# Optimization experiments

Hardware: AMD Instinct MI355X
Metric: run time of the kernel (lower is better)

## Reference

```python
import jax, jax.numpy as jnp
import numpy as np
from jax import lax

S, T, I, H = 50, 2048, 64, 256  # num_series, seq_len, input_size, hidden_size

def _xavier(key, shape):
    fan_in, fan_out = shape[-1], shape[-2]
    b = np.sqrt(6.0 / (fan_in + fan_out)).astype(np.float32)
    return jax.random.uniform(key, shape, jnp.float32, -b, b)

def setup_inputs() -> dict:
    key = jax.random.key(0)
    ks = jax.random.split(key, 6)
    return {
        "input_data": jax.random.normal(ks[0], (S, T, 1 + I), jnp.float32),
        "hidden": jnp.zeros((S, H), jnp.float32),
        "fixed_effects": jax.random.normal(ks[1], (S, T), jnp.float32),
        "W_ih": _xavier(ks[2], (S, H, I)),
        "W_hh": _xavier(ks[3], (S, H, H)),
        "b_ih": jnp.zeros((S, H), jnp.float32),
        "b_hh": jnp.zeros((S, H), jnp.float32),
        "W_lin": _xavier(ks[4], (S, 1, H)),
        "b_lin": jnp.zeros((S, 1), jnp.float32),
        "gaussian_likelihood": 1,
        "prediction": 0,
    }

def reference(input_data, hidden, fixed_effects, W_ih, W_hh, b_ih, b_hh, W_lin, b_lin, gaussian_likelihood, prediction):
    z = input_data[:, :, 0]          # [S, T] targets
    x = input_data[:, :, 1:]         # [S, T, I] RNN inputs

    # All 50 per-series Elman RNNs run as one batched scan over time.
    def step(h, x_t):                # h: [S, H], x_t: [S, I]
        h = jnp.tanh(jnp.einsum('shi,si->sh', W_ih, x_t) + b_ih
                     + jnp.einsum('shg,sg->sh', W_hh, h) + b_hh)
        return h, h

    xs = jnp.swapaxes(x, 0, 1)       # [T, S, I]
    _, hs = lax.scan(step, hidden, xs)
    rnn_out = jnp.swapaxes(hs, 0, 1)  # [S, T, H]

    # Per-series linear head (output_size=1) then abs -> sigma [S, T]
    sig = jnp.einsum('sth,sh->st', rnn_out, W_lin[:, 0, :]) + b_lin
    sigma = jnp.abs(sig)

    if prediction == 0:
        # Gaussian log-likelihood: log N(z-f; 0, sigma) - log N(0; 0, sigma)
        # = -(z - f)^2 / (2 sigma^2), summed over all elements.
        diff = z - fixed_effects
        log_lik = jnp.sum(-(diff * diff) / (2.0 * sigma * sigma))
        return (log_lik, sigma)
    else:
        # r ~ N(0, sigma) elementwise, u = f + r, softmax over time axis.
        eps = jax.random.normal(jax.random.key(1), sigma.shape, sigma.dtype)
        u = fixed_effects + sigma * eps
        return jax.nn.softmax(u, axis=1)
```

## Files before the change

kernel.cpp:

```cpp
#include <hip/hip_runtime.h>
#include <cmath>

#define S_CNT 50
#define T_CNT 2048
#define I_DIM 64
#define H_DIM 256
#define CHK   8
#define NCHK  (T_CNT / CHK)

typedef float vf2 __attribute__((ext_vector_type(2)));

__device__ __forceinline__ float fast_tanh(float x) {
    float e = __expf(2.0f * x);
    return 1.0f - __fdividef(2.0f, e + 1.0f);
}

__device__ __forceinline__ vf2 pkfma(vf2 a, vf2 b, vf2 c) {
#if __has_builtin(__builtin_elementwise_fma)
    return __builtin_elementwise_fma(a, b, c);
#else
    vf2 r; r.x = fmaf(a.x, b.x, c.x); r.y = fmaf(a.y, b.y, c.y); return r;
#endif
}

__device__ __forceinline__ float fma4(const float4 w, const float4 h, float a) {
    a = fmaf(w.x, h.x, a);
    a = fmaf(w.y, h.y, a);
    a = fmaf(w.z, h.z, a);
    a = fmaf(w.w, h.w, a);
    return a;
}

template <int CTRL>
__device__ __forceinline__ float dpp_xadd(float x) {
    const int xi = __float_as_int(x);
    const int yi = __builtin_amdgcn_update_dpp(xi, xi, CTRL, 0xF, 0xF, false);
    return x + __int_as_float(yi);
}

__device__ __forceinline__ void lds_barrier() {
    __builtin_amdgcn_sched_barrier(0);
    asm volatile("s_waitcnt lgkmcnt(0)");
    __builtin_amdgcn_s_barrier();
    __builtin_amdgcn_sched_barrier(0);
}

__launch_bounds__(256, 4)
__global__ void precompute_u_kernel(const float* __restrict__ input_data,
                                    const float* __restrict__ W_ih,
                                    const float* __restrict__ b_ih,
                                    const float* __restrict__ b_hh,
                                    float* __restrict__ U)
{
    const int s  = blockIdx.x;
    const int tb = blockIdx.y;
    const int j  = threadIdx.x;

    float4 w[16];
    const float4* wrow =
        reinterpret_cast<const float4*>(W_ih + ((size_t)s * H_DIM + j) * I_DIM);
#pragma unroll
    for (int k = 0; k < 16; ++k) w[k] = wrow[k];
    const float bsum = b_ih[s * H_DIM + j] + b_hh[s * H_DIM + j];

    __shared__ float xs[32][I_DIM];
    const float* inb = input_data + (size_t)s * T_CNT * 65;
    float* Ub = U + (size_t)s * T_CNT * H_DIM;

    const int t0 = tb * 32;
    for (int idx = j; idx < 32 * I_DIM; idx += 256) {
        const int row = idx >> 6, col = idx & 63;
        xs[row][col] = inb[(size_t)(t0 + row) * 65 + 1 + col];
    }
    __syncthreads();
    for (int tt = 0; tt < 32; ++tt) {
        const float4* xv = reinterpret_cast<const float4*>(&xs[tt][0]);
        float a0 = bsum, a1 = 0.f, a2 = 0.f, a3 = 0.f;
#pragma unroll
        for (int k = 0; k < 16; k += 4) {
            a0 = fma4(w[k],     xv[k],     a0);
            a1 = fma4(w[k + 1], xv[k + 1], a1);
            a2 = fma4(w[k + 2], xv[k + 2], a2);
            a3 = fma4(w[k + 3], xv[k + 3], a3);
        }
        Ub[(size_t)(t0 + tt) * H_DIM + j] = (a0 + a1) + (a2 + a3);
    }
}

__global__
__launch_bounds__(512)
__attribute__((amdgpu_waves_per_eu(1, 2)))
void rnn_main9(const float* __restrict__ hidden,
               const float* __restrict__ W_hh,
               float* __restrict__ U)
{
    const int s    = blockIdx.x;
    const int tid  = threadIdx.x;
    const int g    = tid >> 3;
    const int p    = tid & 7;

    const int s1 = (p ^ (p >> 2)) & 1;
    const int s2 = (p ^ (p >> 1)) & 1;
    const int jr = s1 + 2 * s2;
    const int jown = 4 * g + jr;

    __shared__ __align__(16) float hA[H_DIM];
    __shared__ __align__(16) float hB[H_DIM];

    if (tid < H_DIM) hA[tid] = hidden[s * H_DIM + tid];

    vf2 w2[4][16];
#pragma unroll
    for (int r = 0; r < 4; ++r) {
        const float4* wrow = reinterpret_cast<const float4*>(
            W_hh + ((size_t)s * H_DIM + 4 * g + r) * H_DIM);
#pragma unroll
        for (int m = 0; m < 8; ++m) {
            const float4 wv = wrow[8 * m + p];
            w2[r][2 * m]     = vf2{wv.x, wv.y};
            w2[r][2 * m + 1] = vf2{wv.z, wv.w};
        }
    }

    float* Ub = U + (size_t)s * T_CNT * H_DIM;
    float* us = Ub + jown;

    const float* u0 = Ub + jown;
    float cu0 = u0[0 * H_DIM], cu1 = u0[1 * H_DIM];
    float cu2 = u0[2 * H_DIM], cu3 = u0[3 * H_DIM];
    float cu4 = u0[4 * H_DIM], cu5 = u0[5 * H_DIM];
    float cu6 = u0[6 * H_DIM], cu7 = u0[7 * H_DIM];
    const float* up = Ub + jown + CHK * H_DIM;

    const bool wsel = (p < 4);
    const bool sel1 = (s1 != 0);
    const bool sel2 = (s2 != 0);

    __syncthreads();

#define RNN_STEP(HRD, HWR, UVAL)                                              \
    {                                                                         \
        const float4* hv = reinterpret_cast<const float4*>(HRD);              \
        vf2 a0 = vf2{0.f, 0.f}, b0 = vf2{0.f, 0.f};                           \
        vf2 a1 = vf2{0.f, 0.f}, b1 = vf2{0.f, 0.f};                           \
        vf2 a2 = vf2{0.f, 0.f}, b2 = vf2{0.f, 0.f};                           \
        vf2 a3 = vf2{0.f, 0.f}, b3 = vf2{0.f, 0.f};                           \
        _Pragma("unroll")                                                     \
        for (int m = 0; m < 8; ++m) {                                         \
            const float4 h4 = hv[8 * m + p];                                  \
            const vf2 hlo = vf2{h4.x, h4.y};                                  \
            const vf2 hhi = vf2{h4.z, h4.w};                                  \
            a0 = pkfma(w2[0][2 * m], hlo, a0);                                \
            b0 = pkfma(w2[0][2 * m + 1], hhi, b0);                            \
            a1 = pkfma(w2[1][2 * m], hlo, a1);                                \
            b1 = pkfma(w2[1][2 * m + 1], hhi, b1);                            \
            a2 = pkfma(w2[2][2 * m], hlo, a2);                                \
            b2 = pkfma(w2[2][2 * m + 1], hhi, b2);                            \
            a3 = pkfma(w2[3][2 * m], hlo, a3);                                \
            b3 = pkfma(w2[3][2 * m + 1], hhi, b3);                            \
        }                                                                     \
        const vf2 s0v = a0 + b0, s1v = a1 + b1;                               \
        const vf2 s2v = a2 + b2, s3v = a3 + b3;                               \
        const float d0 = s0v.x + s0v.y, d1 = s1v.x + s1v.y;                   \
        const float d2 = s2v.x + s2v.y, d3 = s3v.x + s3v.y;                   \
                                                         \
        const float e0 = dpp_xadd<0xB1>(d0);                                  \
        const float e1 = dpp_xadd<0xB1>(d1);                                  \
        const float e2 = dpp_xadd<0xB1>(d2);                                  \
        const float e3 = dpp_xadd<0xB1>(d3);                                  \
                        \
        const float c0 = sel1 ? e1 : e0;                                      \
        const float c1 = sel1 ? e3 : e2;                                      \
                                                         \
        const float f0 = dpp_xadd<0x4E>(c0);                                  \
        const float f1 = dpp_xadd<0x4E>(c1);                                  \
                               \
        const float gg = sel2 ? f1 : f0;                                      \
                  \
        const float fr = dpp_xadd<0x141>(gg);                                 \
        const float hval = fast_tanh(fr + (UVAL));                            \
        if (wsel) { (HWR)[jown] = hval; *us = hval; }                         \
        us += H_DIM;                                                          \
        lds_barrier();                                                        \
    }

    for (int c = 0; c < NCHK; ++c) {
        const float nx0 = up[0 * H_DIM], nx1 = up[1 * H_DIM];
        const float nx2 = up[2 * H_DIM], nx3 = up[3 * H_DIM];
        const float nx4 = up[4 * H_DIM], nx5 = up[5 * H_DIM];
        const float nx6 = up[6 * H_DIM], nx7 = up[7 * H_DIM];

        RNN_STEP(hA, hB, cu0)
        RNN_STEP(hB, hA, cu1)
        RNN_STEP(hA, hB, cu2)
        RNN_STEP(hB, hA, cu3)
        RNN_STEP(hA, hB, cu4)
        RNN_STEP(hB, hA, cu5)
        RNN_STEP(hA, hB, cu6)
        RNN_STEP(hB, hA, cu7)

        cu0 = nx0; cu1 = nx1; cu2 = nx2; cu3 = nx3;
        cu4 = nx4; cu5 = nx5; cu6 = nx6; cu7 = nx7;
        if (c < NCHK - 2) up += CHK * H_DIM;
    }
#undef RNN_STEP
}

__launch_bounds__(256, 4)
__global__ void finalize_kernel(const float* __restrict__ input_data,
                                const float* __restrict__ fe,
                                const float* __restrict__ W_lin,
                                const float* __restrict__ b_lin,
                                const float* __restrict__ H,
                                float* __restrict__ out)
{
    const int s    = blockIdx.x;
    const int tb   = blockIdx.y;
    const int tid  = threadIdx.x;
    const int wave = tid >> 6;
    const int lane = tid & 63;

    const float4 wl =
        reinterpret_cast<const float4*>(W_lin + s * H_DIM)[lane];
    const float blin = b_lin[s];
    const float* Hb  = H + (size_t)s * T_CNT * H_DIM;
    const float* inb = input_data + (size_t)s * T_CNT * 65;
    const float* feb = fe + (size_t)s * T_CNT;
    float* sig_out   = out + 1 + (size_t)s * T_CNT;

    float ll = 0.f;
    for (int i = 0; i < 128; ++i) {
        const int t = tb * 512 + 4 * i + wave;
        const float4 h4 =
            reinterpret_cast<const float4*>(Hb + (size_t)t * H_DIM)[lane];
        float d = fma4(wl, h4, 0.f);
#pragma unroll
        for (int m = 1; m <= 32; m <<= 1) d += __shfl_xor(d, m);
        const float sigma = fabsf(d + blin);
        if (lane == 0) {
            sig_out[t] = sigma;
            const float diff = inb[(size_t)t * 65] - feb[t];
            ll -= (diff * diff) / (2.f * sigma * sigma);
        }
    }
    __shared__ float red[4];
    if (lane == 0) red[wave] = ll;
    __syncthreads();
    if (tid == 0) atomicAdd(out, (red[0] + red[1]) + (red[2] + red[3]));
}

__launch_bounds__(1024, 4)
__global__ void rnn_fallback_kernel(const float* __restrict__ input_data,
                                    const float* __restrict__ hidden,
                                    const float* __restrict__ fe,
                                    const float* __restrict__ W_ih,
                                    const float* __restrict__ W_hh,
                                    const float* __restrict__ b_ih,
                                    const float* __restrict__ b_hh,
                                    const float* __restrict__ W_lin,
                                    const float* __restrict__ b_lin,
                                    float* __restrict__ out)
{
    const int s    = blockIdx.x;
    const int tid  = threadIdx.x;
    const int j    = tid >> 2;
    const int q    = tid & 3;
    const int lane = tid & 63;
    const int wv   = tid >> 6;

    __shared__ float hbuf[2][H_DIM];
    __shared__ float zbuf[T_CNT];
    __shared__ float febuf[T_CNT];
    __shared__ float wlin_lds[H_DIM];
    __shared__ float wsum[2][16];
    __shared__ float xbuf[64][I_DIM];

    const float* in_base = input_data + (size_t)s * T_CNT * 65;
    const float* fe_base = fe + (size_t)s * T_CNT;

    for (int t = tid; t < T_CNT; t += 1024) {
        zbuf[t]  = in_base[(size_t)t * 65];
        febuf[t] = fe_base[t];
    }
    if (tid < H_DIM) {
        hbuf[1][tid]  = hidden[s * H_DIM + tid];
        wlin_lds[tid] = W_lin[s * H_DIM + tid];
    }

    float4 w[16];
    {
        const float4* wrow =
            reinterpret_cast<const float4*>(W_hh + ((size_t)s * H_DIM + j) * H_DIM);
#pragma unroll
        for (int m = 0; m < 16; ++m) w[m] = wrow[4 * m + q];
    }
    float4 wx[4];
    {
        const float4* wxrow =
            reinterpret_cast<const float4*>(W_ih + ((size_t)s * H_DIM + j) * I_DIM);
#pragma unroll
        for (int m = 0; m < 4; ++m) wx[m] = wxrow[4 * m + q];
    }
    const float badd = b_ih[s * H_DIM + j] + b_hh[s * H_DIM + j];
    const float blin = b_lin[s];
    float* sig_out = out + 1 + (size_t)s * T_CNT;

    float ll = 0.f, sv_prev = 0.f;
    __syncthreads();

    for (int c = 0; c < T_CNT / 64; ++c) {
        for (int idx = tid; idx < 64 * I_DIM; idx += 1024) {
            const int row = idx >> 6, col = idx & 63;
            xbuf[row][col] = in_base[(size_t)(c * 64 + row) * 65 + 1 + col];
        }
        __syncthreads();
        for (int tt = 0; tt < 64; ++tt) {
            const int t  = c * 64 + tt;
            const int rp = (t + 1) & 1;
            {
                float sv = sv_prev;
                sv += __shfl_xor(sv, 4);
                sv += __shfl_xor(sv, 8);
                sv += __shfl_xor(sv, 16);
                sv += __shfl_xor(sv, 32);
                if (lane == 0) wsum[(t - 1) & 1][wv] = sv;
            }
            if (tid == 0 && t >= 2) {
                const int tm = t - 2;
                const float* wp = wsum[tm & 1];
                float sg = (((wp[0] + wp[1]) + (wp[2] + wp[3])) +
                            ((wp[4] + wp[5]) + (wp[6] + wp[7]))) +
                           (((wp[8] + wp[9]) + (wp[10] + wp[11])) +
                            ((wp[12] + wp[13]) + (wp[14] + wp[15]))) + blin;
                const float sigma = fabsf(sg);
                sig_out[tm] = sigma;
                const float diff = zbuf[tm] - febuf[tm];
                ll -= (diff * diff) / (2.f * sigma * sigma);
            }
            const float4* hv = reinterpret_cast<const float4*>(&hbuf[rp][0]);
            float a0 = 0.f, a1 = 0.f, a2 = 0.f, a3 = 0.f;
#pragma unroll
            for (int m = 0; m < 16; m += 4) {
                a0 = fma4(w[m],     hv[4 * (m + 0) + q], a0);
                a1 = fma4(w[m + 1], hv[4 * (m + 1) + q], a1);
                a2 = fma4(w[m + 2], hv[4 * (m + 2) + q], a2);
                a3 = fma4(w[m + 3], hv[4 * (m + 3) + q], a3);
            }
            const float4* xv = reinterpret_cast<const float4*>(&xbuf[tt][0]);
#pragma unroll
            for (int m = 0; m < 4; ++m) a0 = fma4(wx[m], xv[4 * m + q], a0);

            float dot = (a0 + a1) + (a2 + a3);
            dot += __shfl_xor(dot, 1);
            dot += __shfl_xor(dot, 2);
            const float h = fast_tanh(dot + badd);
            if (q == 0) hbuf[t & 1][j] = h;
            sv_prev = h * wlin_lds[j];
            __syncthreads();
        }
        __syncthreads();
    }
    {
        float sv = sv_prev;
        sv += __shfl_xor(sv, 4);
        sv += __shfl_xor(sv, 8);
        sv += __shfl_xor(sv, 16);
        sv += __shfl_xor(sv, 32);
        if (lane == 0) wsum[(T_CNT - 1) & 1][wv] = sv;
    }
    __syncthreads();
    if (tid == 0) {
        for (int tm = T_CNT - 2; tm < T_CNT; ++tm) {
            const float* wp = wsum[tm & 1];
            float sg = (((wp[0] + wp[1]) + (wp[2] + wp[3])) +
                        ((wp[4] + wp[5]) + (wp[6] + wp[7]))) +
                       (((wp[8] + wp[9]) + (wp[10] + wp[11])) +
                        ((wp[12] + wp[13]) + (wp[14] + wp[15]))) + blin;
            const float sigma = fabsf(sg);
            sig_out[tm] = sigma;
            const float diff = zbuf[tm] - febuf[tm];
            ll -= (diff * diff) / (2.f * sigma * sigma);
        }
        atomicAdd(out, ll);
    }
}

extern "C" void kernel_launch(void* const* d_in, const int* in_sizes, int n_in,
                              void* d_out, int out_size, void* d_ws, size_t ws_size,
                              hipStream_t stream) {
    (void)in_sizes; (void)n_in; (void)out_size;
    const float* input_data = (const float*)d_in[0];
    const float* hidden     = (const float*)d_in[1];
    const float* fe         = (const float*)d_in[2];
    const float* W_ih       = (const float*)d_in[3];
    const float* W_hh       = (const float*)d_in[4];
    const float* b_ih       = (const float*)d_in[5];
    const float* b_hh       = (const float*)d_in[6];
    const float* W_lin      = (const float*)d_in[7];
    const float* b_lin      = (const float*)d_in[8];
    float* out = (float*)d_out;

    hipMemsetAsync(d_out, 0, sizeof(float), stream);

    const size_t u_bytes = (size_t)S_CNT * T_CNT * H_DIM * sizeof(float);

    if (ws_size >= u_bytes) {
        float* U = (float*)d_ws;
        precompute_u_kernel<<<dim3(S_CNT, 64), 256, 0, stream>>>(
            input_data, W_ih, b_ih, b_hh, U);
        rnn_main9<<<dim3(S_CNT), dim3(512), 0, stream>>>(hidden, W_hh, U);
        finalize_kernel<<<dim3(S_CNT, 4), 256, 0, stream>>>(
            input_data, fe, W_lin, b_lin, U, out);
    } else {
        rnn_fallback_kernel<<<dim3(S_CNT), dim3(1024), 0, stream>>>(
            input_data, hidden, fe, W_ih, W_hh, b_ih, b_hh, W_lin, b_lin, out);
    }
}
```

Measured before the change: 1.530 ms.

## Split recurrent dot product across 16 lanes per row group with 1024 threads

The recurrent kernel now uses 1024 threads per series, with each 4-row group split across 16 lanes instead of 8. That halves the per-thread dot-product length and the register footprint of the W_hh slice, and adds one more DPP reduction stage (row_half_mirror-style 0x140) to combine across 16 lanes. The intent is to shorten the serial per-timestep critical path, at the cost of an extra cross-lane step and more waves synchronizing at each barrier. The precompute kernel is also changed so each block processes 128 timesteps in four 32-step chunks, giving fewer blocks that each reuse their loaded W_ih registers longer.

```diff
diff --git a/kernel.cpp b/kernel.cpp
--- a/kernel.cpp
+++ b/kernel.cpp
@@ -7,6 +7,7 @@
 #define H_DIM 256
 #define CHK   8
 #define NCHK  (T_CNT / CHK)
+#define NTHR  1024
 
 typedef float vf2 __attribute__((ext_vector_type(2)));
 
@@ -67,37 +68,40 @@
     const float* inb = input_data + (size_t)s * T_CNT * 65;
     float* Ub = U + (size_t)s * T_CNT * H_DIM;
 
-    const int t0 = tb * 32;
-    for (int idx = j; idx < 32 * I_DIM; idx += 256) {
-        const int row = idx >> 6, col = idx & 63;
-        xs[row][col] = inb[(size_t)(t0 + row) * 65 + 1 + col];
-    }
-    __syncthreads();
-    for (int tt = 0; tt < 32; ++tt) {
-        const float4* xv = reinterpret_cast<const float4*>(&xs[tt][0]);
-        float a0 = bsum, a1 = 0.f, a2 = 0.f, a3 = 0.f;
-#pragma unroll
-        for (int k = 0; k < 16; k += 4) {
-            a0 = fma4(w[k],     xv[k],     a0);
-            a1 = fma4(w[k + 1], xv[k + 1], a1);
-            a2 = fma4(w[k + 2], xv[k + 2], a2);
-            a3 = fma4(w[k + 3], xv[k + 3], a3);
-        }
-        Ub[(size_t)(t0 + tt) * H_DIM + j] = (a0 + a1) + (a2 + a3);
+    for (int c = 0; c < 4; ++c) {
+        const int t0 = tb * 128 + c * 32;
+        __syncthreads();
+        for (int idx = j; idx < 32 * I_DIM; idx += 256) {
+            const int row = idx >> 6, col = idx & 63;
+            xs[row][col] = inb[(size_t)(t0 + row) * 65 + 1 + col];
+        }
+        __syncthreads();
+        for (int tt = 0; tt < 32; ++tt) {
+            const float4* xv = reinterpret_cast<const float4*>(&xs[tt][0]);
+            float a0 = bsum, a1 = 0.f, a2 = 0.f, a3 = 0.f;
+#pragma unroll
+            for (int k = 0; k < 16; k += 4) {
+                a0 = fma4(w[k],     xv[k],     a0);
+                a1 = fma4(w[k + 1], xv[k + 1], a1);
+                a2 = fma4(w[k + 2], xv[k + 2], a2);
+                a3 = fma4(w[k + 3], xv[k + 3], a3);
+            }
+            Ub[(size_t)(t0 + tt) * H_DIM + j] = (a0 + a1) + (a2 + a3);
+        }
     }
 }
 
 __global__
-__launch_bounds__(512)
-__attribute__((amdgpu_waves_per_eu(1, 2)))
-void rnn_main9(const float* __restrict__ hidden,
-               const float* __restrict__ W_hh,
-               float* __restrict__ U)
+__launch_bounds__(NTHR)
+__attribute__((amdgpu_waves_per_eu(4, 4)))
+void rnn_main10(const float* __restrict__ hidden,
+                const float* __restrict__ W_hh,
+                float* __restrict__ U)
 {
     const int s    = blockIdx.x;
     const int tid  = threadIdx.x;
-    const int g    = tid >> 3;
-    const int p    = tid & 7;
+    const int g    = tid >> 4;
+    const int p    = tid & 15;
 
     const int s1 = (p ^ (p >> 2)) & 1;
     const int s2 = (p ^ (p >> 1)) & 1;
@@ -109,14 +113,14 @@
 
     if (tid < H_DIM) hA[tid] = hidden[s * H_DIM + tid];
 
-    vf2 w2[4][16];
+    vf2 w2[4][8];
 #pragma unroll
     for (int r = 0; r < 4; ++r) {
         const float4* wrow = reinterpret_cast<const float4*>(
             W_hh + ((size_t)s * H_DIM + 4 * g + r) * H_DIM);
 #pragma unroll
-        for (int m = 0; m < 8; ++m) {
-            const float4 wv = wrow[8 * m + p];
+        for (int m = 0; m < 4; ++m) {
+            const float4 wv = wrow[16 * m + p];
             w2[r][2 * m]     = vf2{wv.x, wv.y};
             w2[r][2 * m + 1] = vf2{wv.z, wv.w};
         }
@@ -146,8 +150,8 @@
         vf2 a2 = vf2{0.f, 0.f}, b2 = vf2{0.f, 0.f};                           \
         vf2 a3 = vf2{0.f, 0.f}, b3 = vf2{0.f, 0.f};                           \
         _Pragma("unroll")                                                     \
-        for (int m = 0; m < 8; ++m) {                                         \
-            const float4 h4 = hv[8 * m + p];                                  \
+        for (int m = 0; m < 4; ++m) {                                         \
+            const float4 h4 = hv[16 * m + p];                                 \
             const vf2 hlo = vf2{h4.x, h4.y};                                  \
             const vf2 hhi = vf2{h4.z, h4.w};                                  \
             a0 = pkfma(w2[0][2 * m], hlo, a0);                                \
@@ -161,23 +165,24 @@
         }                                                                     \
         const vf2 s0v = a0 + b0, s1v = a1 + b1;                               \
         const vf2 s2v = a2 + b2, s3v = a3 + b3;                               \
-        const float d0 = s0v.x + s0v.y, d1 = s1v.x + s1v.y;                   \
-        const float d2 = s2v.x + s2v.y, d3 = s3v.x + s3v.y;                   \
+        float d0 = s0v.x + s0v.y, d1 = s1v.x + s1v.y;                         \
+        float d2 = s2v.x + s2v.y, d3 = s3v.x + s3v.y;                         \
                                                          \
-        const float e0 = dpp_xadd<0xB1>(d0);                                  \
-        const float e1 = dpp_xadd<0xB1>(d1);                                  \
-        const float e2 = dpp_xadd<0xB1>(d2);                                  \
-        const float e3 = dpp_xadd<0xB1>(d3);                                  \
-                        \
-        const float c0 = sel1 ? e1 : e0;                                      \
-        const float c1 = sel1 ? e3 : e2;                                      \
+        d0 = dpp_xadd<0xB1>(d0);                                              \
+        d1 = dpp_xadd<0xB1>(d1);                                              \
+        d2 = dpp_xadd<0xB1>(d2);                                              \
+        d3 = dpp_xadd<0xB1>(d3);                                              \
+                                                    \
+        float c0 = sel1 ? d1 : d0;                                            \
+        float c1 = sel1 ? d3 : d2;                                            \
                                                          \
-        const float f0 = dpp_xadd<0x4E>(c0);                                  \
-        const float f1 = dpp_xadd<0x4E>(c1);                                  \
-                               \
-        const float gg = sel2 ? f1 : f0;                                      \
-                  \
-        const float fr = dpp_xadd<0x141>(gg);                                 \
+        c0 = dpp_xadd<0x4E>(c0);                                              \
+        c1 = dpp_xadd<0x4E>(c1);                                              \
+                                                    \
+        float gg = sel2 ? c1 : c0;                                            \
+        \
+        gg = dpp_xadd<0x141>(gg);                                             \
+        const float fr = dpp_xadd<0x140>(gg);                                 \
         const float hval = fast_tanh(fr + (UVAL));                            \
         if (wsel) { (HWR)[jown] = hval; *us = hval; }                         \
         us += H_DIM;                                                          \
@@ -406,9 +411,9 @@
 
     if (ws_size >= u_bytes) {
         float* U = (float*)d_ws;
-        precompute_u_kernel<<<dim3(S_CNT, 64), 256, 0, stream>>>(
+        precompute_u_kernel<<<dim3(S_CNT, 16), 256, 0, stream>>>(
             input_data, W_ih, b_ih, b_hh, U);
-        rnn_main9<<<dim3(S_CNT), dim3(512), 0, stream>>>(hidden, W_hh, U);
+        rnn_main10<<<dim3(S_CNT), dim3(NTHR), 0, stream>>>(hidden, W_hh, U);
         finalize_kernel<<<dim3(S_CNT, 4), 256, 0, stream>>>(
             input_data, fe, W_lin, b_lin, U, out);
     } else {
```

New measurement: 1.918 ms. +25.4%, slower.

## Halve recurrent block to 256 threads with 8 rows per thread group

Applied to the files above, without the earlier changes.

The sequential RNN kernel now runs 256 threads per series instead of 512. Each 8-lane group owns 8 hidden rows rather than 4, and a three-level DPP butterfly with selects gives every lane exactly one output, so no lanes sit idle on the write. The aim is to cut per-step barrier cost and LDS reads of h by using fewer waves, at the price of twice the FMA work per thread and 256 weight registers per thread, which risks spilling. The input-projection kernel also now loops over 4 time chunks per block, using 16 blocks per series instead of 64.

```diff
diff --git a/kernel.cpp b/kernel.cpp
--- a/kernel.cpp
+++ b/kernel.cpp
@@ -67,53 +67,56 @@
     const float* inb = input_data + (size_t)s * T_CNT * 65;
     float* Ub = U + (size_t)s * T_CNT * H_DIM;
 
-    const int t0 = tb * 32;
-    for (int idx = j; idx < 32 * I_DIM; idx += 256) {
-        const int row = idx >> 6, col = idx & 63;
-        xs[row][col] = inb[(size_t)(t0 + row) * 65 + 1 + col];
-    }
-    __syncthreads();
-    for (int tt = 0; tt < 32; ++tt) {
-        const float4* xv = reinterpret_cast<const float4*>(&xs[tt][0]);
-        float a0 = bsum, a1 = 0.f, a2 = 0.f, a3 = 0.f;
-#pragma unroll
-        for (int k = 0; k < 16; k += 4) {
-            a0 = fma4(w[k],     xv[k],     a0);
-            a1 = fma4(w[k + 1], xv[k + 1], a1);
-            a2 = fma4(w[k + 2], xv[k + 2], a2);
-            a3 = fma4(w[k + 3], xv[k + 3], a3);
-        }
-        Ub[(size_t)(t0 + tt) * H_DIM + j] = (a0 + a1) + (a2 + a3);
+    for (int c = 0; c < 4; ++c) {
+        const int t0 = tb * 128 + c * 32;
+        __syncthreads();
+        for (int idx = j; idx < 32 * I_DIM; idx += 256) {
+            const int row = idx >> 6, col = idx & 63;
+            xs[row][col] = inb[(size_t)(t0 + row) * 65 + 1 + col];
+        }
+        __syncthreads();
+        for (int tt = 0; tt < 32; ++tt) {
+            const float4* xv = reinterpret_cast<const float4*>(&xs[tt][0]);
+            float a0 = bsum, a1 = 0.f, a2 = 0.f, a3 = 0.f;
+#pragma unroll
+            for (int k = 0; k < 16; k += 4) {
+                a0 = fma4(w[k],     xv[k],     a0);
+                a1 = fma4(w[k + 1], xv[k + 1], a1);
+                a2 = fma4(w[k + 2], xv[k + 2], a2);
+                a3 = fma4(w[k + 3], xv[k + 3], a3);
+            }
+            Ub[(size_t)(t0 + tt) * H_DIM + j] = (a0 + a1) + (a2 + a3);
+        }
     }
 }
 
 __global__
-__launch_bounds__(512)
-__attribute__((amdgpu_waves_per_eu(1, 2)))
-void rnn_main9(const float* __restrict__ hidden,
-               const float* __restrict__ W_hh,
-               float* __restrict__ U)
+__launch_bounds__(256)
+__attribute__((amdgpu_waves_per_eu(1, 1)))
+void rnn_main11(const float* __restrict__ hidden,
+                const float* __restrict__ W_hh,
+                float* __restrict__ U)
 {
-    const int s    = blockIdx.x;
-    const int tid  = threadIdx.x;
-    const int g    = tid >> 3;
-    const int p    = tid & 7;
+    const int s   = blockIdx.x;
+    const int tid = threadIdx.x;
+    const int g   = tid >> 3;
+    const int p   = tid & 7;
 
     const int s1 = (p ^ (p >> 2)) & 1;
     const int s2 = (p ^ (p >> 1)) & 1;
-    const int jr = s1 + 2 * s2;
-    const int jown = 4 * g + jr;
+    const int s3 = (p >> 2) & 1;
+    const int jown = 8 * g + s1 + 2 * s2 + 4 * s3;
 
     __shared__ __align__(16) float hA[H_DIM];
     __shared__ __align__(16) float hB[H_DIM];
 
-    if (tid < H_DIM) hA[tid] = hidden[s * H_DIM + tid];
-
-    vf2 w2[4][16];
-#pragma unroll
-    for (int r = 0; r < 4; ++r) {
+    hA[tid] = hidden[s * H_DIM + tid];
+
+    vf2 w2[8][16];
+#pragma unroll
+    for (int r = 0; r < 8; ++r) {
         const float4* wrow = reinterpret_cast<const float4*>(
-            W_hh + ((size_t)s * H_DIM + 4 * g + r) * H_DIM);
+            W_hh + ((size_t)s * H_DIM + 8 * g + r) * H_DIM);
 #pragma unroll
         for (int m = 0; m < 8; ++m) {
             const float4 wv = wrow[8 * m + p];
@@ -132,54 +135,76 @@
     float cu6 = u0[6 * H_DIM], cu7 = u0[7 * H_DIM];
     const float* up = Ub + jown + CHK * H_DIM;
 
-    const bool wsel = (p < 4);
-    const bool sel1 = (s1 != 0);
-    const bool sel2 = (s2 != 0);
+    const bool sb1 = (s1 != 0);
+    const bool sb2 = (s2 != 0);
+    const bool sb3 = (s3 != 0);
 
     __syncthreads();
 
 #define RNN_STEP(HRD, HWR, UVAL)                                              \
     {                                                                         \
         const float4* hv = reinterpret_cast<const float4*>(HRD);              \
-        vf2 a0 = vf2{0.f, 0.f}, b0 = vf2{0.f, 0.f};                           \
-        vf2 a1 = vf2{0.f, 0.f}, b1 = vf2{0.f, 0.f};                           \
-        vf2 a2 = vf2{0.f, 0.f}, b2 = vf2{0.f, 0.f};                           \
-        vf2 a3 = vf2{0.f, 0.f}, b3 = vf2{0.f, 0.f};                           \
+        vf2 aa0 = vf2{0.f, 0.f}, bb0 = vf2{0.f, 0.f};                         \
+        vf2 aa1 = vf2{0.f, 0.f}, bb1 = vf2{0.f, 0.f};                         \
+        vf2 aa2 = vf2{0.f, 0.f}, bb2 = vf2{0.f, 0.f};                         \
+        vf2 aa3 = vf2{0.f, 0.f}, bb3 = vf2{0.f, 0.f};                         \
+        vf2 aa4 = vf2{0.f, 0.f}, bb4 = vf2{0.f, 0.f};                         \
+        vf2 aa5 = vf2{0.f, 0.f}, bb5 = vf2{0.f, 0.f};                         \
+        vf2 aa6 = vf2{0.f, 0.f}, bb6 = vf2{0.f, 0.f};                         \
+        vf2 aa7 = vf2{0.f, 0.f}, bb7 = vf2{0.f, 0.f};                         \
         _Pragma("unroll")                                                     \
         for (int m = 0; m < 8; ++m) {                                         \
             const float4 h4 = hv[8 * m + p];                                  \
             const vf2 hlo = vf2{h4.x, h4.y};                                  \
             const vf2 hhi = vf2{h4.z, h4.w};                                  \
-            a0 = pkfma(w2[0][2 * m], hlo, a0);                                \
-            b0 = pkfma(w2[0][2 * m + 1], hhi, b0);                            \
-            a1 = pkfma(w2[1][2 * m], hlo, a1);                                \
-            b1 = pkfma(w2[1][2 * m + 1], hhi, b1);                            \
-            a2 = pkfma(w2[2][2 * m], hlo, a2);                                \
-            b2 = pkfma(w2[2][2 * m + 1], hhi, b2);                            \
-            a3 = pkfma(w2[3][2 * m], hlo, a3);                                \
-            b3 = pkfma(w2[3][2 * m + 1], hhi, b3);                            \
+            aa0 = pkfma(w2[0][2 * m], hlo, aa0);                              \
+            bb0 = pkfma(w2[0][2 * m + 1], hhi, bb0);                          \
+            aa1 = pkfma(w2[1][2 * m], hlo, aa1);                              \
+            bb1 = pkfma(w2[1][2 * m + 1], hhi, bb1);                          \
+            aa2 = pkfma(w2[2][2 * m], hlo, aa2);                              \
+            bb2 = pkfma(w2[2][2 * m + 1], hhi, bb2);                          \
+            aa3 = pkfma(w2[3][2 * m], hlo, aa3);                              \
+            bb3 = pkfma(w2[3][2 * m + 1], hhi, bb3);                          \
+            aa4 = pkfma(w2[4][2 * m], hlo, aa4);                              \
+            bb4 = pkfma(w2[4][2 * m + 1], hhi, bb4);                          \
+            aa5 = pkfma(w2[5][2 * m], hlo, aa5);                              \
+            bb5 = pkfma(w2[5][2 * m + 1], hhi, bb5);                          \
+            aa6 = pkfma(w2[6][2 * m], hlo, aa6);                              \
+            bb6 = pkfma(w2[6][2 * m + 1], hhi, bb6);                          \
+            aa7 = pkfma(w2[7][2 * m], hlo, aa7);                              \
+            bb7 = pkfma(w2[7][2 * m + 1], hhi, bb7);                          \
         }                                                                     \
-        const vf2 s0v = a0 + b0, s1v = a1 + b1;                               \
-        const vf2 s2v = a2 + b2, s3v = a3 + b3;                               \
-        const float d0 = s0v.x + s0v.y, d1 = s1v.x + s1v.y;                   \
-        const float d2 = s2v.x + s2v.y, d3 = s3v.x + s3v.y;                   \
-                                                         \
-        const float e0 = dpp_xadd<0xB1>(d0);                                  \
-        const float e1 = dpp_xadd<0xB1>(d1);                                  \
-        const float e2 = dpp_xadd<0xB1>(d2);                                  \
-        const float e3 = dpp_xadd<0xB1>(d3);                                  \
-                        \
-        const float c0 = sel1 ? e1 : e0;                                      \
-        const float c1 = sel1 ? e3 : e2;                                      \
-                                                         \
-        const float f0 = dpp_xadd<0x4E>(c0);                                  \
-        const float f1 = dpp_xadd<0x4E>(c1);                                  \
-                               \
-        const float gg = sel2 ? f1 : f0;                                      \
-                  \
-        const float fr = dpp_xadd<0x141>(gg);                                 \
+        const vf2 v0 = aa0 + bb0, v1 = aa1 + bb1;                             \
+        const vf2 v2 = aa2 + bb2, v3 = aa3 + bb3;                             \
+        const vf2 v4 = aa4 + bb4, v5 = aa5 + bb5;                             \
+        const vf2 v6 = aa6 + bb6, v7 = aa7 + bb7;                             \
+        float d0 = v0.x + v0.y, d1 = v1.x + v1.y;                             \
+        float d2 = v2.x + v2.y, d3 = v3.x + v3.y;                             \
+        float d4 = v4.x + v4.y, d5 = v5.x + v5.y;                             \
+        float d6 = v6.x + v6.y, d7 = v7.x + v7.y;                             \
+                            \
+        d0 = dpp_xadd<0xB1>(d0); d1 = dpp_xadd<0xB1>(d1);                     \
+        d2 = dpp_xadd<0xB1>(d2); d3 = dpp_xadd<0xB1>(d3);                     \
+        d4 = dpp_xadd<0xB1>(d4); d5 = dpp_xadd<0xB1>(d5);                     \
+        d6 = dpp_xadd<0xB1>(d6); d7 = dpp_xadd<0xB1>(d7);                     \
+        const float e0 = sb1 ? d1 : d0;                                       \
+        const float e1 = sb1 ? d3 : d2;                                       \
+        const float e2 = sb1 ? d5 : d4;                                       \
+        const float e3 = sb1 ? d7 : d6;                                       \
+                            \
+        const float f0a = dpp_xadd<0x4E>(e0);                                 \
+        const float f1a = dpp_xadd<0x4E>(e1);                                 \
+        const float f2a = dpp_xadd<0x4E>(e2);                                 \
+        const float f3a = dpp_xadd<0x4E>(e3);                                 \
+        const float g0 = sb2 ? f1a : f0a;                                     \
+        const float g1 = sb2 ? f3a : f2a;                                     \
+                     \
+        const float h0 = dpp_xadd<0x141>(g0);                                 \
+        const float h1 = dpp_xadd<0x141>(g1);                                 \
+        const float fr = sb3 ? h1 : h0;                                       \
         const float hval = fast_tanh(fr + (UVAL));                            \
-        if (wsel) { (HWR)[jown] = hval; *us = hval; }                         \
+        (HWR)[jown] = hval;                                                   \
+        *us = hval;                                                           \
         us += H_DIM;                                                          \
         lds_barrier();                                                        \
     }
@@ -406,9 +431,9 @@
 
     if (ws_size >= u_bytes) {
         float* U = (float*)d_ws;
-        precompute_u_kernel<<<dim3(S_CNT, 64), 256, 0, stream>>>(
+        precompute_u_kernel<<<dim3(S_CNT, 16), 256, 0, stream>>>(
             input_data, W_ih, b_ih, b_hh, U);
-        rnn_main9<<<dim3(S_CNT), dim3(512), 0, stream>>>(hidden, W_hh, U);
+        rnn_main11<<<dim3(S_CNT), dim3(256), 0, stream>>>(hidden, W_hh, U);
         finalize_kernel<<<dim3(S_CNT, 4), 256, 0, stream>>>(
             input_data, fe, W_lin, b_lin, U, out);
     } else {
```

After: 3.576 ms. 2.34x slower.
